# Performance work log

Measured on AMD Instinct MI355X. Metric: run time of the kernel, lower is better.

Reference implementation:

```python
import jax, jax.numpy as jnp
import numpy as np

NEG = -1000000000.0

def setup_inputs() -> dict:
    key = jax.random.key(0)
    k1, k2 = jax.random.split(key)
    N, D, K = 8192, 4096, 64
    z = jax.random.normal(k1, (N, D), dtype=jnp.float32)
    W = jax.random.normal(k2, (K, D), dtype=jnp.float32) * (1.0 / np.sqrt(D))
    b = jnp.zeros((K,), dtype=jnp.float32)
    return {"z": z, "W": W, "b": b, "k": 2}

def reference(z, W, b, k):
    # logits: [N, K]
    logits = jnp.einsum('nd,kd->nk', z, W) + b
    _, topk_idx = jax.lax.top_k(logits, k)  # [N, k]
    N = logits.shape[0]
    rows = jnp.arange(N)[:, None]
    mask = jnp.zeros_like(logits).at[rows, topk_idx].set(1.0)
    sparse_logits = logits + NEG * (1.0 - mask)
    alpha = jax.nn.softmax(sparse_logits, axis=-1)
    return alpha
```

## Files before the change

### kernel.cpp

```cpp
#include <hip/hip_runtime.h>
#include <math.h>


typedef short bf16x8 __attribute__((ext_vector_type(8)));
typedef float f32x4  __attribute__((ext_vector_type(4)));

constexpr int D_DIM  = 4096;
constexpr int K_DIM  = 64;
constexpr int BM     = 128;
constexpr int CH     = 64;
constexpr int KQ     = 4;
constexpr int KRANGE = D_DIM / KQ;
constexpr int NCH    = KRANGE / CH;
constexpr int BLOCK  = 512;
constexpr int LSTR   = 72;

__device__ __forceinline__ unsigned short bf16_rne(float f) {
    unsigned int u = __float_as_uint(f);
    u += 0x7FFFu + ((u >> 16) & 1u);
    return (unsigned short)(u >> 16);
}
__device__ __forceinline__ float bf16_f(unsigned short h) {
    return __uint_as_float(((unsigned int)h) << 16);
}

__global__ __launch_bounds__(BLOCK, 2) void gemm_mfma(
    const float* __restrict__ z, const float* __restrict__ W,
    float* __restrict__ part, int N)
{
    __shared__ __align__(16) unsigned short Az[3][BM][LSTR];
    __shared__ __align__(16) unsigned short Bw[3][K_DIM][LSTR];

    const int tid  = threadIdx.x;
    const int lane = tid & 63;
    const int wv   = tid >> 6;
    const int m16  = lane & 15;
    const int quad = lane >> 4;

    const int rgrp  = blockIdx.x >> 2;
    const int kq    = blockIdx.x & 3;
    const long m0   = (long)rgrp * BM;
    const int kbase = kq * KRANGE;

    float4 zbuf[4], wbuf[2];
#pragma unroll
    for (int i = 0; i < 4; ++i) {
        int f = tid + i * BLOCK, r = f >> 4, k4 = (f & 15) * 4;
        zbuf[i] = *(const float4*)(z + (m0 + r) * (long)D_DIM + kbase + k4);
    }
#pragma unroll
    for (int i = 0; i < 2; ++i) {
        int f = tid + i * BLOCK, c = f >> 4, k4 = (f & 15) * 4;
        wbuf[i] = *(const float4*)(W + (long)c * D_DIM + kbase + k4);
    }

    f32x4 acc[4];
#pragma unroll
    for (int nt = 0; nt < 4; ++nt) acc[nt] = (f32x4){0.f, 0.f, 0.f, 0.f};

    for (int ch = 0; ch < NCH; ++ch) {
#pragma unroll
        for (int i = 0; i < 4; ++i) {
            int f = tid + i * BLOCK, r = f >> 4, k4 = (f & 15) * 4;
            unsigned short h[4], m[4], l[4];
            const float* p = (const float*)&zbuf[i];
#pragma unroll
            for (int j = 0; j < 4; ++j) {
                h[j] = bf16_rne(p[j]);
                float x1 = p[j] - bf16_f(h[j]);
                m[j] = bf16_rne(x1);
                l[j] = bf16_rne(x1 - bf16_f(m[j]));
            }
            *(ushort4*)&Az[0][r][k4] = make_ushort4(h[0], h[1], h[2], h[3]);
            *(ushort4*)&Az[1][r][k4] = make_ushort4(m[0], m[1], m[2], m[3]);
            *(ushort4*)&Az[2][r][k4] = make_ushort4(l[0], l[1], l[2], l[3]);
        }
#pragma unroll
        for (int i = 0; i < 2; ++i) {
            int f = tid + i * BLOCK, c = f >> 4, k4 = (f & 15) * 4;
            unsigned short h[4], m[4], l[4];
            const float* p = (const float*)&wbuf[i];
#pragma unroll
            for (int j = 0; j < 4; ++j) {
                h[j] = bf16_rne(p[j]);
                float x1 = p[j] - bf16_f(h[j]);
                m[j] = bf16_rne(x1);
                l[j] = bf16_rne(x1 - bf16_f(m[j]));
            }
            *(ushort4*)&Bw[0][c][k4] = make_ushort4(h[0], h[1], h[2], h[3]);
            *(ushort4*)&Bw[1][c][k4] = make_ushort4(m[0], m[1], m[2], m[3]);
            *(ushort4*)&Bw[2][c][k4] = make_ushort4(l[0], l[1], l[2], l[3]);
        }
        __syncthreads();

        if (ch + 1 < NCH) {
            const int k0 = kbase + (ch + 1) * CH;
#pragma unroll
            for (int i = 0; i < 4; ++i) {
                int f = tid + i * BLOCK, r = f >> 4, k4 = (f & 15) * 4;
                zbuf[i] = *(const float4*)(z + (m0 + r) * (long)D_DIM + k0 + k4);
            }
#pragma unroll
            for (int i = 0; i < 2; ++i) {
                int f = tid + i * BLOCK, c = f >> 4, k4 = (f & 15) * 4;
                wbuf[i] = *(const float4*)(W + (long)c * D_DIM + k0 + k4);
            }
        }

        const int mrow = wv * 16 + m16;
#pragma unroll
        for (int ks2 = 0; ks2 < 2; ++ks2) {
            const int ko = ks2 * 32 + quad * 8;
            const bf16x8 ah = *(const bf16x8*)&Az[0][mrow][ko];
            const bf16x8 am = *(const bf16x8*)&Az[1][mrow][ko];
            const bf16x8 al = *(const bf16x8*)&Az[2][mrow][ko];
#pragma unroll
            for (int nt = 0; nt < 4; ++nt) {
                const int ncol = nt * 16 + m16;
                const bf16x8 bh = *(const bf16x8*)&Bw[0][ncol][ko];
                const bf16x8 bm = *(const bf16x8*)&Bw[1][ncol][ko];
                const bf16x8 bl = *(const bf16x8*)&Bw[2][ncol][ko];
                f32x4 a = acc[nt];
                a = __builtin_amdgcn_mfma_f32_16x16x32_bf16(al, bh, a, 0, 0, 0);
                a = __builtin_amdgcn_mfma_f32_16x16x32_bf16(am, bm, a, 0, 0, 0);
                a = __builtin_amdgcn_mfma_f32_16x16x32_bf16(ah, bl, a, 0, 0, 0);
                a = __builtin_amdgcn_mfma_f32_16x16x32_bf16(am, bh, a, 0, 0, 0);
                a = __builtin_amdgcn_mfma_f32_16x16x32_bf16(ah, bm, a, 0, 0, 0);
                a = __builtin_amdgcn_mfma_f32_16x16x32_bf16(ah, bh, a, 0, 0, 0);
                acc[nt] = a;
            }
        }
        __syncthreads();
    }

#pragma unroll
    for (int nt = 0; nt < 4; ++nt) {
#pragma unroll
        for (int r = 0; r < 4; ++r) {
            long row = m0 + wv * 16 + quad * 4 + r;
            int  col = nt * 16 + m16;
            part[((long)kq * N + row) * K_DIM + col] = acc[nt][r];
        }
    }
}

constexpr int RG2  = 32;
constexpr int BLK2 = 256;

__global__ __launch_bounds__(BLK2) void reduce_topk(
    const float* __restrict__ part, const float* __restrict__ bias,
    float* __restrict__ out, int N)
{
    __shared__ float lg[RG2][K_DIM + 1];
    __shared__ float sa1[RG2], sa2[RG2];
    __shared__ int   si1[RG2], si2[RG2];

    const int tid = threadIdx.x;
    const long r0 = (long)blockIdx.x * RG2;

#pragma unroll
    for (int i = 0; i < (RG2 * K_DIM) / (BLK2 * 4); ++i) {
        int f = tid + i * BLK2, r = f >> 4, c4 = (f & 15) * 4;
        float4 s = *(const float4*)(part + (r0 + r) * K_DIM + c4);
#pragma unroll
        for (int q = 1; q < KQ; ++q) {
            const float4 v = *(const float4*)(part + ((long)q * N + r0 + r) * K_DIM + c4);
            s.x += v.x; s.y += v.y; s.z += v.z; s.w += v.w;
        }
        const float4 bv = *(const float4*)(bias + c4);
        lg[r][c4 + 0] = s.x + bv.x;
        lg[r][c4 + 1] = s.y + bv.y;
        lg[r][c4 + 2] = s.z + bv.z;
        lg[r][c4 + 3] = s.w + bv.w;
    }
    __syncthreads();

    if (tid < RG2) {
        float m1 = -INFINITY, m2 = -INFINITY;
        int i1 = 0, i2 = 0;
        for (int j = 0; j < K_DIM; ++j) {
            float v = lg[tid][j];
            if (v > m1)      { m2 = m1; i2 = i1; m1 = v; i1 = j; }
            else if (v > m2) { m2 = v; i2 = j; }
        }
        float e2  = expf(m2 - m1);
        float inv = 1.f / (1.f + e2);
        sa1[tid] = inv; sa2[tid] = e2 * inv;
        si1[tid] = i1;  si2[tid] = i2;
    }
    __syncthreads();

    float* obase = out + r0 * K_DIM;
#pragma unroll
    for (int i = 0; i < (RG2 * K_DIM) / (BLK2 * 4); ++i) {
        int f = tid + i * BLK2, r = f >> 4, j = (f & 15) * 4;
        int i1 = si1[r], i2 = si2[r];
        float a1 = sa1[r], a2 = sa2[r];
        float4 v;
        v.x = (j + 0 == i1) ? a1 : ((j + 0 == i2) ? a2 : 0.f);
        v.y = (j + 1 == i1) ? a1 : ((j + 1 == i2) ? a2 : 0.f);
        v.z = (j + 2 == i1) ? a1 : ((j + 2 == i2) ? a2 : 0.f);
        v.w = (j + 3 == i1) ? a1 : ((j + 3 == i2) ? a2 : 0.f);
        *(float4*)(obase + (long)r * K_DIM + j) = v;
    }
}

extern "C" void kernel_launch(void* const* d_in, const int* in_sizes, int n_in,
                              void* d_out, int out_size, void* d_ws, size_t ws_size,
                              hipStream_t stream) {
    const float* z = (const float*)d_in[0];
    const float* W = (const float*)d_in[1];
    const float* b = (const float*)d_in[2];
    float* out  = (float*)d_out;
    float* part = (float*)d_ws;
    const int N = in_sizes[0] / D_DIM;
    gemm_mfma  <<<dim3((N / BM) * KQ), dim3(BLOCK), 0, stream>>>(z, W, part, N);
    reduce_topk<<<dim3(N / RG2),       dim3(BLK2), 0, stream>>>(part, b, out, N);
}
```

Baseline: 219.3 us.

## Replace 3-limb bf16 split GEMM with scaled 2-limb fp16 split

Switches the fp32-emulating GEMM from a three-way bf16 decomposition (6 MFMAs per tile) to a two-way fp16 decomposition with the low limb scaled by 2048 (3 MFMAs per tile, cross terms in a separate accumulator). The row tile shrinks from 128 to 64, which doubles the grid. Waves are split across M and N halves, and launch bounds now target 4 blocks per CU. This roughly halves MFMA work, LDS traffic and conversion cost, but fp16 range and precision could flip top-2 selections on near-tied logits, and W rows are reloaded by twice as many blocks.

```diff
diff --git a/kernel.cpp b/kernel.cpp
--- a/kernel.cpp
+++ b/kernel.cpp
@@ -2,12 +2,13 @@
 #include <math.h>
 
 
-typedef short bf16x8 __attribute__((ext_vector_type(8)));
-typedef float f32x4  __attribute__((ext_vector_type(4)));
+typedef _Float16 f16x8 __attribute__((ext_vector_type(8)));
+typedef _Float16 f16x4 __attribute__((ext_vector_type(4)));
+typedef float    f32x4 __attribute__((ext_vector_type(4)));
 
 constexpr int D_DIM  = 4096;
 constexpr int K_DIM  = 64;
-constexpr int BM     = 128;
+constexpr int BM     = 64;
 constexpr int CH     = 64;
 constexpr int KQ     = 4;
 constexpr int KRANGE = D_DIM / KQ;
@@ -15,25 +16,18 @@
 constexpr int BLOCK  = 512;
 constexpr int LSTR   = 72;
 
-__device__ __forceinline__ unsigned short bf16_rne(float f) {
-    unsigned int u = __float_as_uint(f);
-    u += 0x7FFFu + ((u >> 16) & 1u);
-    return (unsigned short)(u >> 16);
-}
-__device__ __forceinline__ float bf16_f(unsigned short h) {
-    return __uint_as_float(((unsigned int)h) << 16);
-}
-
-__global__ __launch_bounds__(BLOCK, 2) void gemm_mfma(
+__global__ __launch_bounds__(BLOCK, 4) void gemm_f16limb(
     const float* __restrict__ z, const float* __restrict__ W,
     float* __restrict__ part, int N)
 {
-    __shared__ __align__(16) unsigned short Az[3][BM][LSTR];
-    __shared__ __align__(16) unsigned short Bw[3][K_DIM][LSTR];
+    __shared__ __align__(16) _Float16 Az[2][BM][LSTR];
+    __shared__ __align__(16) _Float16 Bw[2][K_DIM][LSTR];
 
     const int tid  = threadIdx.x;
     const int lane = tid & 63;
     const int wv   = tid >> 6;
+    const int mt   = wv >> 1;
+    const int nh   = wv & 1;
     const int m16  = lane & 15;
     const int quad = lane >> 4;
 
@@ -42,104 +36,81 @@
     const long m0   = (long)rgrp * BM;
     const int kbase = kq * KRANGE;
 
-    float4 zbuf[4], wbuf[2];
-#pragma unroll
-    for (int i = 0; i < 4; ++i) {
-        int f = tid + i * BLOCK, r = f >> 4, k4 = (f & 15) * 4;
-        zbuf[i] = *(const float4*)(z + (m0 + r) * (long)D_DIM + kbase + k4);
-    }
+    float4 zb[2], wb[2];
 #pragma unroll
     for (int i = 0; i < 2; ++i) {
-        int f = tid + i * BLOCK, c = f >> 4, k4 = (f & 15) * 4;
-        wbuf[i] = *(const float4*)(W + (long)c * D_DIM + kbase + k4);
+        int f = tid + i * BLOCK, r = f >> 4, k4 = (f & 15) * 4;
+        zb[i] = *(const float4*)(z + (m0 + r) * (long)D_DIM + kbase + k4);
+        wb[i] = *(const float4*)(W + (long)r * D_DIM + kbase + k4);
     }
 
-    f32x4 acc[4];
+    f32x4 acch[2], accl[2];
 #pragma unroll
-    for (int nt = 0; nt < 4; ++nt) acc[nt] = (f32x4){0.f, 0.f, 0.f, 0.f};
+    for (int t = 0; t < 2; ++t) {
+        acch[t] = (f32x4){0.f, 0.f, 0.f, 0.f};
+        accl[t] = (f32x4){0.f, 0.f, 0.f, 0.f};
+    }
 
     for (int ch = 0; ch < NCH; ++ch) {
 #pragma unroll
-        for (int i = 0; i < 4; ++i) {
+        for (int i = 0; i < 2; ++i) {
             int f = tid + i * BLOCK, r = f >> 4, k4 = (f & 15) * 4;
-            unsigned short h[4], m[4], l[4];
-            const float* p = (const float*)&zbuf[i];
+            const float* pz = (const float*)&zb[i];
+            const float* pw = (const float*)&wb[i];
+            f16x4 zh, zl, wh, wl;
 #pragma unroll
             for (int j = 0; j < 4; ++j) {
-                h[j] = bf16_rne(p[j]);
-                float x1 = p[j] - bf16_f(h[j]);
-                m[j] = bf16_rne(x1);
-                l[j] = bf16_rne(x1 - bf16_f(m[j]));
+                _Float16 h = (_Float16)pz[j];
+                zh[j] = h;
+                zl[j] = (_Float16)((pz[j] - (float)h) * 2048.0f);
+                _Float16 g = (_Float16)pw[j];
+                wh[j] = g;
+                wl[j] = (_Float16)((pw[j] - (float)g) * 2048.0f);
             }
-            *(ushort4*)&Az[0][r][k4] = make_ushort4(h[0], h[1], h[2], h[3]);
-            *(ushort4*)&Az[1][r][k4] = make_ushort4(m[0], m[1], m[2], m[3]);
-            *(ushort4*)&Az[2][r][k4] = make_ushort4(l[0], l[1], l[2], l[3]);
-        }
-#pragma unroll
-        for (int i = 0; i < 2; ++i) {
-            int f = tid + i * BLOCK, c = f >> 4, k4 = (f & 15) * 4;
-            unsigned short h[4], m[4], l[4];
-            const float* p = (const float*)&wbuf[i];
-#pragma unroll
-            for (int j = 0; j < 4; ++j) {
-                h[j] = bf16_rne(p[j]);
-                float x1 = p[j] - bf16_f(h[j]);
-                m[j] = bf16_rne(x1);
-                l[j] = bf16_rne(x1 - bf16_f(m[j]));
-            }
-            *(ushort4*)&Bw[0][c][k4] = make_ushort4(h[0], h[1], h[2], h[3]);
-            *(ushort4*)&Bw[1][c][k4] = make_ushort4(m[0], m[1], m[2], m[3]);
-            *(ushort4*)&Bw[2][c][k4] = make_ushort4(l[0], l[1], l[2], l[3]);
+            *(f16x4*)&Az[0][r][k4] = zh;
+            *(f16x4*)&Az[1][r][k4] = zl;
+            *(f16x4*)&Bw[0][r][k4] = wh;
+            *(f16x4*)&Bw[1][r][k4] = wl;
         }
         __syncthreads();
 
         if (ch + 1 < NCH) {
             const int k0 = kbase + (ch + 1) * CH;
 #pragma unroll
-            for (int i = 0; i < 4; ++i) {
+            for (int i = 0; i < 2; ++i) {
                 int f = tid + i * BLOCK, r = f >> 4, k4 = (f & 15) * 4;
-                zbuf[i] = *(const float4*)(z + (m0 + r) * (long)D_DIM + k0 + k4);
-            }
-#pragma unroll
-            for (int i = 0; i < 2; ++i) {
-                int f = tid + i * BLOCK, c = f >> 4, k4 = (f & 15) * 4;
-                wbuf[i] = *(const float4*)(W + (long)c * D_DIM + k0 + k4);
+                zb[i] = *(const float4*)(z + (m0 + r) * (long)D_DIM + k0 + k4);
+                wb[i] = *(const float4*)(W + (long)r * D_DIM + k0 + k4);
             }
         }
 
-        const int mrow = wv * 16 + m16;
+        const int mrow = mt * 16 + m16;
 #pragma unroll
-        for (int ks2 = 0; ks2 < 2; ++ks2) {
-            const int ko = ks2 * 32 + quad * 8;
-            const bf16x8 ah = *(const bf16x8*)&Az[0][mrow][ko];
-            const bf16x8 am = *(const bf16x8*)&Az[1][mrow][ko];
-            const bf16x8 al = *(const bf16x8*)&Az[2][mrow][ko];
+        for (int ks = 0; ks < 2; ++ks) {
+            const int ko = ks * 32 + quad * 8;
+            const f16x8 ah = *(const f16x8*)&Az[0][mrow][ko];
+            const f16x8 al = *(const f16x8*)&Az[1][mrow][ko];
 #pragma unroll
-            for (int nt = 0; nt < 4; ++nt) {
-                const int ncol = nt * 16 + m16;
-                const bf16x8 bh = *(const bf16x8*)&Bw[0][ncol][ko];
-                const bf16x8 bm = *(const bf16x8*)&Bw[1][ncol][ko];
-                const bf16x8 bl = *(const bf16x8*)&Bw[2][ncol][ko];
-                f32x4 a = acc[nt];
-                a = __builtin_amdgcn_mfma_f32_16x16x32_bf16(al, bh, a, 0, 0, 0);
-                a = __builtin_amdgcn_mfma_f32_16x16x32_bf16(am, bm, a, 0, 0, 0);
-                a = __builtin_amdgcn_mfma_f32_16x16x32_bf16(ah, bl, a, 0, 0, 0);
-                a = __builtin_amdgcn_mfma_f32_16x16x32_bf16(am, bh, a, 0, 0, 0);
-                a = __builtin_amdgcn_mfma_f32_16x16x32_bf16(ah, bm, a, 0, 0, 0);
-                a = __builtin_amdgcn_mfma_f32_16x16x32_bf16(ah, bh, a, 0, 0, 0);
-                acc[nt] = a;
+            for (int t = 0; t < 2; ++t) {
+                const int ncol = (nh * 2 + t) * 16 + m16;
+                const f16x8 bh = *(const f16x8*)&Bw[0][ncol][ko];
+                const f16x8 bl = *(const f16x8*)&Bw[1][ncol][ko];
+                accl[t] = __builtin_amdgcn_mfma_f32_16x16x32_f16(al, bh, accl[t], 0, 0, 0);
+                accl[t] = __builtin_amdgcn_mfma_f32_16x16x32_f16(ah, bl, accl[t], 0, 0, 0);
+                acch[t] = __builtin_amdgcn_mfma_f32_16x16x32_f16(ah, bh, acch[t], 0, 0, 0);
             }
         }
         __syncthreads();
     }
 
 #pragma unroll
-    for (int nt = 0; nt < 4; ++nt) {
+    for (int t = 0; t < 2; ++t) {
 #pragma unroll
         for (int r = 0; r < 4; ++r) {
-            long row = m0 + wv * 16 + quad * 4 + r;
-            int  col = nt * 16 + m16;
-            part[((long)kq * N + row) * K_DIM + col] = acc[nt][r];
+            long row = m0 + mt * 16 + quad * 4 + r;
+            int  col = (nh * 2 + t) * 16 + m16;
+            part[((long)kq * N + row) * K_DIM + col] =
+                acch[t][r] + accl[t][r] * 4.8828125e-4f;
         }
     }
 }
@@ -214,6 +185,6 @@
     float* out  = (float*)d_out;
     float* part = (float*)d_ws;
     const int N = in_sizes[0] / D_DIM;
-    gemm_mfma  <<<dim3((N / BM) * KQ), dim3(BLOCK), 0, stream>>>(z, W, part, N);
-    reduce_topk<<<dim3(N / RG2),       dim3(BLK2), 0, stream>>>(part, b, out, N);
+    gemm_f16limb<<<dim3((N / BM) * KQ), dim3(BLOCK), 0, stream>>>(z, W, part, N);
+    reduce_topk <<<dim3(N / RG2),       dim3(BLK2), 0, stream>>>(part, b, out, N);
 }
```

Result: faster. 212.4 us (-3.1%).
